# Performance work log

Hardware: AMD Instinct MI355X
Metric: run time of the kernel (lower is better)

The kernel has to match this reference:

```python
import jax, jax.numpy as jnp
import numpy as np
import math

B, T = 16, 512
P = 256          # num_memory_positions
E = 128          # embedding_dim
NB = 4           # num_beings
K = 4            # attention_radius
TEMP = 8.0       # attention_temperature
PHI = 1.618033988749895


def setup_inputs() -> dict:
    key = jax.random.key(0)
    ks = jax.random.split(key, 8)
    x = jax.random.normal(ks[0], (B, T, 8), jnp.float32)
    W_in = jax.random.normal(ks[1], (8, E), jnp.float32) * 0.1
    b_in = jnp.zeros((E,), jnp.float32)
    W_out = jax.random.normal(ks[2], (E, 8), jnp.float32) * 0.1
    b_out = jnp.zeros((8,), jnp.float32)
    W_p = jax.random.normal(ks[3], (E, E), jnp.float32) * (1.0 / np.sqrt(E))
    b_p = jnp.zeros((E,), jnp.float32)
    ptr_dest = jax.random.uniform(ks[4], (NB, P), jnp.float32) * P
    jump_W = jax.random.normal(ks[5], (NB, E), jnp.float32) * 0.1
    jump_b = jnp.zeros((NB,), jnp.float32)
    ctx_strength = jnp.full((NB,), 0.2, jnp.float32)
    pe = np.zeros((NB, E), np.float32)
    for i in range(NB):
        ph = i * PHI
        v = []
        for h in range(1, 9):
            v += [math.sin(h * ph), math.cos(h * ph)]
        pe[i, :16] = v  # phase_embedding padded with zeros to E (E >= 16)
    phase_bias = jnp.asarray(pe)
    seg = P / NB
    pointer_init = jax.random.uniform(ks[6], (NB, B), jnp.float32) * seg + jnp.arange(NB, dtype=jnp.float32)[:, None] * seg
    return dict(x=x, W_in=W_in, b_in=b_in, W_out=W_out, b_out=b_out,
                W_p=W_p, b_p=b_p, ptr_dest=ptr_dest, jump_W=jump_W,
                jump_b=jump_b, ctx_strength=ctx_strength,
                phase_bias=phase_bias, pointer_init=pointer_init)


def _forward(x, W_in, b_in, W_out, b_out, W_p, b_p, ptr_dest, jump_W,
             jump_b, ctx_strength, phase_bias, pointer_init):
    offsets = jnp.arange(-K, K + 1)          # [W]
    b_ix = jnp.arange(B)                     # [B]
    half = P / 2.0
    ring0 = jnp.zeros((B, P, E), x.dtype)
    hid0 = jnp.zeros((NB, B, E), x.dtype)

    def step(carry, x_t):
        ring, ptrs, hids = carry
        inp = x_t @ W_in + b_in              # [B,E]
        outs, new_ptrs, new_hids = [], [], []
        for i in range(NB):                  # beings sequential (share ring)
            ptr, hid = ptrs[i], hids[i]
            base = jnp.clip(jnp.floor(ptr).astype(jnp.int32), 0, P - 1)
            idx = (base[:, None] + offsets[None, :]) % P            # [B,W]
            delta = jnp.mod(idx.astype(x_t.dtype) - ptr[:, None] + half, P) - half
            w = jax.nn.softmax(-(delta ** 2) / TEMP, axis=1)         # [B,W]
            nbhd = ring[b_ix[:, None], idx]                          # [B,W,E]
            ctx = jnp.sum(w[..., None] * nbhd, axis=1)               # [B,E]
            comb = inp + jax.nn.sigmoid(ctx_strength[i]) * ctx + 0.1 * phase_bias[i]
            s = jnp.tanh(comb + hid)
            s = jnp.tanh(s @ W_p + b_p)      # depth-1 = 1 processing layer
            ring = ring.at[b_ix[:, None], idx].add(w[..., None] * s[:, None, :])
            cur = jnp.clip(ptr.astype(jnp.int32), 0, P - 1)
            jump_target = ptr_dest[i][cur]                           # [B]
            probs = jax.nn.sigmoid(s @ jump_W[i] + jump_b[i])        # [B]
            hard = (probs > 0.5).astype(s.dtype)
            should_jump = hard - jax.lax.stop_gradient(probs) + probs
            walk = (ptr + 1.0) % P
            new_ptrs.append(jnp.where(should_jump > 0.5, jump_target, walk))
            new_hids.append(s)
            outs.append(s @ W_out + b_out)                           # [B,8]
        out_t = jnp.mean(jnp.stack(outs), axis=0)                    # [B,8] (training-mode mean)
        return (ring, jnp.stack(new_ptrs), jnp.stack(new_hids)), out_t

    _, ys = jax.lax.scan(step, (ring0, pointer_init, hid0), jnp.swapaxes(x, 0, 1))
    return jnp.swapaxes(ys, 0, 1)            # [B,T,8]


def reference(x, W_in, b_in, W_out, b_out, W_p, b_p, ptr_dest, jump_W,
              jump_b, ctx_strength, phase_bias, pointer_init):
    return _forward(x, W_in, b_in, W_out, b_out, W_p, b_p, ptr_dest,
                    jump_W, jump_b, ctx_strength, phase_bias, pointer_init)
```

## Files before the change

kernel.cpp:

```cpp
#include <hip/hip_runtime.h>
#include <cmath>

namespace {
constexpr int B_ = 16, T_ = 512, P_ = 256, E_ = 128, NB_ = 4, K_ = 4;
constexpr int THREADS_ = 512;
constexpr int RS_ = 132;

__device__ __forceinline__ float rcpf(float x) { return __builtin_amdgcn_rcpf(x); }
__device__ __forceinline__ float fast_tanh(float x) {
    float a = fabsf(x);
    float t = __expf(-2.0f * a);
    float r = 1.0f - 2.0f * t * rcpf(1.0f + t);
    return copysignf(r, x);
}

__device__ __forceinline__ void lgkm_barrier() {
    __builtin_amdgcn_sched_barrier(0);
    asm volatile("s_waitcnt lgkmcnt(0)\n\ts_barrier" ::: "memory");
    __builtin_amdgcn_sched_barrier(0);
}

template<int CTRL>
__device__ __forceinline__ float dpp_addf(float v) {
    const int s = __builtin_amdgcn_update_dpp(0, __float_as_int(v), CTRL, 0xF, 0xF, true);
    return v + __int_as_float(s);
}
template<int Q>
__device__ __forceinline__ float dpp_bcast4(float v) {
    const int s = __builtin_amdgcn_update_dpp(0, __float_as_int(v), Q * 0x55, 0xF, 0xF, true);
    return __int_as_float(s);
}
__device__ __forceinline__ float pl16_sum(float v) {
#if __has_builtin(__builtin_amdgcn_permlane16_swap)
    const unsigned u = __float_as_uint(v);
    const auto r = __builtin_amdgcn_permlane16_swap(u, u, false, false);
    return __uint_as_float(r[0]) + __uint_as_float(r[1]);
#else
    return v + __shfl_xor(v, 16);
#endif
}
__device__ __forceinline__ float pl32_sum(float v) {
#if __has_builtin(__builtin_amdgcn_permlane32_swap)
    const unsigned u = __float_as_uint(v);
    const auto r = __builtin_amdgcn_permlane32_swap(u, u, false, false);
    return __uint_as_float(r[0]) + __uint_as_float(r[1]);
#else
    return v + __shfl_xor(v, 32);
#endif
}
__device__ __forceinline__ float redkq8(float v) {
    v = dpp_addf<0x128>(v);
    v = pl16_sum(v);
    v = pl32_sum(v);
    return v;
}
__device__ __forceinline__ float redpair(float v) {
    v = dpp_addf<0xB1>(v);
    v = dpp_addf<0x4E>(v);
    v = dpp_addf<0x141>(v);
    return v;
}
__device__ __forceinline__ float sel8f(int kq, float w0, float w1, float w2, float w3,
                                       float w4, float w5, float w6, float w7) {
    const float a = (kq & 1) ? w1 : w0;
    const float b = (kq & 1) ? w3 : w2;
    const float c = (kq & 1) ? w5 : w4;
    const float d = (kq & 1) ? w7 : w6;
    const float e = (kq & 2) ? b : a;
    const float f = (kq & 2) ? d : c;
    return (kq & 4) ? f : e;
}
}

__global__ __launch_bounds__(512, 1)
void swarm_ring_kernel(const float* __restrict__ x,
                       const float* __restrict__ W_in,
                       const float* __restrict__ b_in,
                       const float* __restrict__ W_out,
                       const float* __restrict__ b_out,
                       const float* __restrict__ W_p,
                       const float* __restrict__ b_p,
                       const float* __restrict__ ptr_dest,
                       const float* __restrict__ jump_W,
                       const float* __restrict__ jump_b,
                       const float* __restrict__ ctx_strength,
                       const float* __restrict__ phase_bias,
                       const float* __restrict__ pointer_init,
                       float* __restrict__ out)
{
    __shared__ alignas(16) float  ring[P_ * RS_];
    __shared__ alignas(16) float4 s4[136];
    __shared__ alignas(16) float  sbuf[2][160];
    __shared__ alignas(16) float  red[32];
    __shared__ alignas(16) float  hist[16][132];
    __shared__ alignas(16) float  wout_s[8][132];

    const int tid = threadIdx.x;
    const int b   = blockIdx.x;
    const int w   = tid >> 6;
    const int l   = tid & 63;
    const int s_  = l & 7;
    const int kq  = l >> 3;
    const int e0  = ((w << 3) | s_) << 1;

    for (int k4 = tid; k4 < P_ * RS_ / 4; k4 += THREADS_)
        ((float4*)ring)[k4] = make_float4(0.f, 0.f, 0.f, 0.f);
    for (int idx = tid; idx < 8 * E_; idx += THREADS_) {
        const int m = idx >> 7, ee = idx & 127;
        wout_s[m][ee] = W_out[ee * 8 + m] * 0.25f;
    }

    float2 wp2[16];
    #pragma unroll
    for (int kk = 0; kk < 16; ++kk)
        wp2[kk] = *(const float2*)(W_p + (kq * 16 + kk) * E_ + e0);

    float2 wi2[8];
    #pragma unroll
    for (int k = 0; k < 8; ++k)
        wi2[k] = *(const float2*)(W_in + k * E_ + e0);

    const float2 bin2 = *(const float2*)(b_in + e0);
    const float2 bp2  = *(const float2*)(b_p + e0);
    const float  bout_m = b_out[tid & 7];

    float2 pb2[NB_], jw2[NB_], hid2[NB_];
    float  sigc[NB_], jb_r[NB_], ptrv[NB_];
    #pragma unroll
    for (int i = 0; i < NB_; ++i) {
        const float2 pb = *(const float2*)(phase_bias + i * E_ + e0);
        pb2[i] = make_float2(0.1f * pb.x, 0.1f * pb.y);
        jw2[i] = *(const float2*)(jump_W + i * E_ + e0);
        sigc[i] = 1.0f / (1.0f + __expf(-ctx_strength[i]));
        jb_r[i] = jump_b[i];
        hid2[i] = make_float2(0.f, 0.f);
        ptrv[i] = pointer_init[i * B_ + b];
    }

    const float* xb = x + (size_t)b * T_ * 8;
    float xt[8];
    {
        float4 a0 = ((const float4*)xb)[0], a1 = ((const float4*)xb)[1];
        xt[0]=a0.x; xt[1]=a0.y; xt[2]=a0.z; xt[3]=a0.w;
        xt[4]=a1.x; xt[5]=a1.y; xt[6]=a1.z; xt[7]=a1.w;
    }

    const float Cw1 = 0.8824969f, Cw2 = 0.60653066f, Cw3 = 0.32465247f, Cw4 = 0.13533528f;
    const float Dw1 = 0.7788008f, Dw2 = 0.36787944f, Dw3 = 0.105399225f, Dw4 = 0.018315639f;

    __syncthreads();

    for (int t = 0; t < T_; ++t) {
        int   baseA[NB_];
        float fA[NB_], psinv[NB_], jt[NB_], wgt[NB_][9];
        #pragma unroll
        for (int i = 0; i < NB_; ++i) {
            const float p = ptrv[i];
            const int base = (int)p;
            baseA[i] = base;
            jt[i] = ptr_dest[i * P_ + base];
            const float f = p - (float)base;
            fA[i] = f;
            const float r  = __expf(0.25f * f);
            const float r2 = r * r, r3 = r2 * r, r4 = r2 * r2;
            const float ri = rcpf(r), ri2 = ri * ri, ri3 = ri2 * ri, ri4 = ri2 * ri2;
            const float p0 = Cw4*ri4, p1 = Cw3*ri3, p2 = Cw2*ri2, p3 = Cw1*ri, p4 = 1.0f,
                        p5 = Cw1*r,  p6 = Cw2*r2,  p7 = Cw3*r3,  p8 = Cw4*r4;
            const float sum = ((p0+p1)+(p2+p3)) + ((p4+p5)+(p6+p7)) + p8;
            const float inv = rcpf(sum);
            psinv[i] = inv;
            wgt[i][0]=p0*inv; wgt[i][1]=p1*inv; wgt[i][2]=p2*inv; wgt[i][3]=p3*inv;
            wgt[i][4]=p4*inv; wgt[i][5]=p5*inv; wgt[i][6]=p6*inv; wgt[i][7]=p7*inv;
            wgt[i][8]=p8*inv;
        }

        int ddm[NB_][NB_];
        bool overlap = false;
        #pragma unroll
        for (int j = 1; j < NB_; ++j)
            #pragma unroll
            for (int i = 0; i < j; ++i) {
                const int dd = ((baseA[j] - baseA[i] + 128) & 255) - 128;
                ddm[j][i] = dd;
                overlap = overlap || (dd >= -8 && dd <= 8);
            }

        float  ws[NB_], w8[NB_];
        float2 ctxp2[NB_];
        #pragma unroll
        for (int i = 0; i < NB_; ++i) {
            ws[i] = sel8f(kq, wgt[i][0], wgt[i][1], wgt[i][2], wgt[i][3],
                              wgt[i][4], wgt[i][5], wgt[i][6], wgt[i][7]);
            w8[i] = wgt[i][8];
            const int r0 = (baseA[i] + kq - K_) & (P_ - 1);
            const float2 g0 = *(const float2*)(ring + r0 * RS_ + e0);
            float cx = ws[i] * g0.x;
            float cy = ws[i] * g0.y;
            if (kq == 0) {
                const int r2 = (baseA[i] + K_) & (P_ - 1);
                const float2 g2 = *(const float2*)(ring + r2 * RS_ + e0);
                cx = fmaf(w8[i], g2.x, cx);
                cy = fmaf(w8[i], g2.y, cy);
            }
            ctxp2[i] = make_float2(redkq8(cx), redkq8(cy));
        }

        float2 inp2 = bin2;
        #pragma unroll
        for (int k = 0; k < 8; ++k) {
            inp2.x = fmaf(xt[k], wi2[k].x, inp2.x);
            inp2.y = fmaf(xt[k], wi2[k].y, inp2.y);
        }

        float xtn[8];
        if (t + 1 < T_) {
            float4 a0 = ((const float4*)(xb + (t + 1) * 8))[0];
            float4 a1 = ((const float4*)(xb + (t + 1) * 8))[1];
            xtn[0]=a0.x; xtn[1]=a0.y; xtn[2]=a0.z; xtn[3]=a0.w;
            xtn[4]=a1.x; xtn[5]=a1.y; xtn[6]=a1.z; xtn[7]=a1.w;
        } else {
            #pragma unroll
            for (int k = 0; k < 8; ++k) xtn[k] = 0.f;
        }

        float2 sv2[NB_];

        if (!overlap) {
            float2 s1v[NB_];
            #pragma unroll
            for (int j = 0; j < NB_; ++j) {
                s1v[j].x = fast_tanh(fmaf(sigc[j], ctxp2[j].x, inp2.x + pb2[j].x + hid2[j].x));
                s1v[j].y = fast_tanh(fmaf(sigc[j], ctxp2[j].y, inp2.y + pb2[j].y + hid2[j].y));
            }
            if (kq == 0) {
                const int si = 17 * w + (s_ << 1);
                s4[si]     = make_float4(s1v[0].x, s1v[1].x, s1v[2].x, s1v[3].x);
                s4[si + 1] = make_float4(s1v[0].y, s1v[1].y, s1v[2].y, s1v[3].y);
            }
            lgkm_barrier();

            float2 ab0 = make_float2(0.f, 0.f), ab1 = ab0, ab2 = ab0, ab3 = ab0;
            const float4* sp = s4 + kq * 17;
            #pragma unroll
            for (int kk = 0; kk < 16; ++kk) {
                const float4 sq = sp[kk];
                const float2 w2 = wp2[kk];
                ab0.x = fmaf(sq.x, w2.x, ab0.x); ab0.y = fmaf(sq.x, w2.y, ab0.y);
                ab1.x = fmaf(sq.y, w2.x, ab1.x); ab1.y = fmaf(sq.y, w2.y, ab1.y);
                ab2.x = fmaf(sq.z, w2.x, ab2.x); ab2.y = fmaf(sq.z, w2.y, ab2.y);
                ab3.x = fmaf(sq.w, w2.x, ab3.x); ab3.y = fmaf(sq.w, w2.y, ab3.y);
            }
            sv2[0] = make_float2(fast_tanh(redkq8(ab0.x) + bp2.x), fast_tanh(redkq8(ab0.y) + bp2.y));
            sv2[1] = make_float2(fast_tanh(redkq8(ab1.x) + bp2.x), fast_tanh(redkq8(ab1.y) + bp2.y));
            sv2[2] = make_float2(fast_tanh(redkq8(ab2.x) + bp2.x), fast_tanh(redkq8(ab2.y) + bp2.y));
            sv2[3] = make_float2(fast_tanh(redkq8(ab3.x) + bp2.x), fast_tanh(redkq8(ab3.y) + bp2.y));
            #pragma unroll
            for (int j = 0; j < NB_; ++j) hid2[j] = sv2[j];

            #pragma unroll
            for (int j = 0; j < NB_; ++j) {
                const float2 s = sv2[j];
                const int r0 = (baseA[j] + kq - K_) & (P_ - 1);
                float2* q0 = (float2*)(ring + r0 * RS_ + e0);
                float2 v0 = *q0;
                v0.x = fmaf(ws[j], s.x, v0.x); v0.y = fmaf(ws[j], s.y, v0.y);
                *q0 = v0;
                if (kq == 0) {
                    const int r2 = (baseA[j] + K_) & (P_ - 1);
                    float2* q2 = (float2*)(ring + r2 * RS_ + e0);
                    float2 v2 = *q2;
                    v2.x = fmaf(w8[j], s.x, v2.x); v2.y = fmaf(w8[j], s.y, v2.y);
                    *q2 = v2;
                }
            }
        } else {
            float coefm[NB_][NB_];
            #pragma unroll
            for (int j = 1; j < NB_; ++j) {
                #pragma unroll
                for (int i = 0; i < j; ++i) {
                    const int dd = ddm[j][i];
                    float c = 0.f;
                    if (dd >= -8 && dd <= 8) {
                        const float A = (float)dd - fA[i];
                        const float s  = __expf(-0.25f * (A - fA[j]));
                        const float G  = __expf(0.125f * (fA[i] * fA[i] - A * A));
                        const float s2p = s * s, s3p = s2p * s, s4p = s2p * s2p;
                        const float si = rcpf(s), si2 = si * si, si3 = si2 * si, si4 = si2 * si2;
                        float acc = 0.f;
                        acc += (dd >= 0)              ? Dw4 * si4 : 0.f;
                        acc += (dd >= -1 && dd <= 7)  ? Dw3 * si3 : 0.f;
                        acc += (dd >= -2 && dd <= 6)  ? Dw2 * si2 : 0.f;
                        acc += (dd >= -3 && dd <= 5)  ? Dw1 * si  : 0.f;
                        acc += (dd >= -4 && dd <= 4)  ? 1.0f      : 0.f;
                        acc += (dd >= -5 && dd <= 3)  ? Dw1 * s   : 0.f;
                        acc += (dd >= -6 && dd <= 2)  ? Dw2 * s2p : 0.f;
                        acc += (dd >= -7 && dd <= 1)  ? Dw3 * s3p : 0.f;
                        acc += (dd <= 0)              ? Dw4 * s4p : 0.f;
                        c = psinv[i] * psinv[j] * G * acc;
                    }
                    coefm[j][i] = c;
                }
            }

            #pragma unroll
            for (int j = 0; j < NB_; ++j) {
                float2 ctx = ctxp2[j];
                #pragma unroll
                for (int i = 0; i < j; ++i) {
                    ctx.x = fmaf(coefm[j][i], sv2[i].x, ctx.x);
                    ctx.y = fmaf(coefm[j][i], sv2[i].y, ctx.y);
                }
                float2 s1;
                s1.x = fast_tanh(fmaf(sigc[j], ctx.x, inp2.x + pb2[j].x + hid2[j].x));
                s1.y = fast_tanh(fmaf(sigc[j], ctx.y, inp2.y + pb2[j].y + hid2[j].y));
                if (kq == 0) {
                    const int pf = 20 * w + (s_ << 1);
                    *(float2*)(&sbuf[j & 1][pf]) = s1;
                }
                lgkm_barrier();

                const float4* sp4 = (const float4*)(&sbuf[j & 1][0]);
                float ax = 0.f, ay = 0.f;
                #pragma unroll
                for (int m = 0; m < 4; ++m) {
                    const float4 sq = sp4[5 * kq + m];
                    const float2 wa = wp2[4*m+0], wb = wp2[4*m+1];
                    const float2 wc = wp2[4*m+2], wd = wp2[4*m+3];
                    ax = fmaf(sq.x, wa.x, ax); ay = fmaf(sq.x, wa.y, ay);
                    ax = fmaf(sq.y, wb.x, ax); ay = fmaf(sq.y, wb.y, ay);
                    ax = fmaf(sq.z, wc.x, ax); ay = fmaf(sq.z, wc.y, ay);
                    ax = fmaf(sq.w, wd.x, ax); ay = fmaf(sq.w, wd.y, ay);
                }
                float2 s2;
                s2.x = fast_tanh(redkq8(ax) + bp2.x);
                s2.y = fast_tanh(redkq8(ay) + bp2.y);
                sv2[j] = s2; hid2[j] = s2;

                const int r0 = (baseA[j] + kq - K_) & (P_ - 1);
                float2* q0 = (float2*)(ring + r0 * RS_ + e0);
                float2 v0 = *q0;
                v0.x = fmaf(ws[j], s2.x, v0.x); v0.y = fmaf(ws[j], s2.y, v0.y);
                *q0 = v0;
                if (kq == 0) {
                    const int r2 = (baseA[j] + K_) & (P_ - 1);
                    float2* q2 = (float2*)(ring + r2 * RS_ + e0);
                    float2 v2 = *q2;
                    v2.x = fmaf(w8[j], s2.x, v2.x); v2.y = fmaf(w8[j], s2.y, v2.y);
                    *q2 = v2;
                }
            }
        }

        {
            float vj0 = fmaf(sv2[0].y, jw2[0].y, sv2[0].x * jw2[0].x);
            float vj1 = fmaf(sv2[1].y, jw2[1].y, sv2[1].x * jw2[1].x);
            float vj2 = fmaf(sv2[2].y, jw2[2].y, sv2[2].x * jw2[2].x);
            float vj3 = fmaf(sv2[3].y, jw2[3].y, sv2[3].x * jw2[3].x);
            vj0 = redpair(vj0); vj1 = redpair(vj1); vj2 = redpair(vj2); vj3 = redpair(vj3);
            if (l == 0)
                ((float4*)red)[w] = make_float4(vj0, vj1, vj2, vj3);
        }

        {
            float2 ssum2;
            ssum2.x = (sv2[0].x + sv2[1].x) + (sv2[2].x + sv2[3].x);
            ssum2.y = (sv2[0].y + sv2[1].y) + (sv2[2].y + sv2[3].y);
            if (kq == 0) *(float2*)(&hist[t & 15][e0]) = ssum2;
        }

        lgkm_barrier();

        {
            float rv = red[l & 31];
            rv = dpp_addf<0x124>(rv);
            rv = dpp_addf<0x128>(rv);
            rv = pl16_sum(rv);
            const float zz0 = dpp_bcast4<0>(rv) + jb_r[0];
            const float zz1 = dpp_bcast4<1>(rv) + jb_r[1];
            const float zz2 = dpp_bcast4<2>(rv) + jb_r[2];
            const float zz3 = dpp_bcast4<3>(rv) + jb_r[3];
            const float zz[4] = { zz0, zz1, zz2, zz3 };
            #pragma unroll
            for (int i = 0; i < NB_; ++i) {
                float np;
                if (zz[i] > 0.0f) np = jt[i];
                else { np = ptrv[i] + 1.0f; if (np >= 256.0f) np -= 256.0f; }
                ptrv[i] = np;
            }
        }

        if ((t & 7) == 7 && tid < 64) {
            const int tt = tid >> 3;
            const int m  = tid & 7;
            const float* hrow = hist[(t - 7 + tt) & 15];
            const float* wrow = wout_s[m];
            float acc = 0.f;
            #pragma unroll
            for (int q = 0; q < 32; ++q) {
                const float4 h4 = ((const float4*)hrow)[q];
                const float4 w4 = ((const float4*)wrow)[q];
                acc += ((h4.x * w4.x + h4.y * w4.y) + (h4.z * w4.z + h4.w * w4.w));
            }
            out[((size_t)b * T_ + (t - 7 + tt)) * 8 + m] = acc + bout_m;
        }

        #pragma unroll
        for (int k = 0; k < 8; ++k) xt[k] = xtn[k];
    }
}

extern "C" void kernel_launch(void* const* d_in, const int* in_sizes, int n_in,
                              void* d_out, int out_size, void* d_ws, size_t ws_size,
                              hipStream_t stream) {
    (void)in_sizes; (void)n_in; (void)out_size; (void)d_ws; (void)ws_size;
    swarm_ring_kernel<<<dim3(B_), dim3(THREADS_), 0, stream>>>(
        (const float*)d_in[0],  (const float*)d_in[1],  (const float*)d_in[2],
        (const float*)d_in[3],  (const float*)d_in[4],  (const float*)d_in[5],
        (const float*)d_in[6],  (const float*)d_in[7],  (const float*)d_in[8],
        (const float*)d_in[9],  (const float*)d_in[10], (const float*)d_in[11],
        (const float*)d_in[12], (float*)d_out);
}
```

Baseline: 2.035 ms.

## Compute W_p projection with bf16x3-split MFMA instead of scalar FMAs

```diff
diff --git a/kernel.cpp b/kernel.cpp
--- a/kernel.cpp
+++ b/kernel.cpp
@@ -5,6 +5,10 @@
 constexpr int B_ = 16, T_ = 512, P_ = 256, E_ = 128, NB_ = 4, K_ = 4;
 constexpr int THREADS_ = 512;
 constexpr int RS_ = 132;
+
+typedef __attribute__((ext_vector_type(8))) short        bf16x8;
+typedef __attribute__((ext_vector_type(4))) float        f32x4;
+typedef __attribute__((ext_vector_type(4))) unsigned int u32x4;
 
 __device__ __forceinline__ float rcpf(float x) { return __builtin_amdgcn_rcpf(x); }
 __device__ __forceinline__ float fast_tanh(float x) {
@@ -18,6 +22,27 @@
     __builtin_amdgcn_sched_barrier(0);
     asm volatile("s_waitcnt lgkmcnt(0)\n\ts_barrier" ::: "memory");
     __builtin_amdgcn_sched_barrier(0);
+}
+
+__device__ __forceinline__ unsigned bf16rn_hi(float x) {
+    const unsigned u = __float_as_uint(x);
+    return (u + 0x7FFFu + ((u >> 16) & 1u)) & 0xFFFF0000u;
+}
+__device__ __forceinline__ void split3_pack(float x, float y,
+                                            unsigned &hp, unsigned &mp, unsigned &lp) {
+    const unsigned xh = bf16rn_hi(x);
+    const float    xr1 = x - __uint_as_float(xh);
+    const unsigned xm = bf16rn_hi(xr1);
+    const float    xr2 = xr1 - __uint_as_float(xm);
+    const unsigned xl = bf16rn_hi(xr2);
+    const unsigned yh = bf16rn_hi(y);
+    const float    yr1 = y - __uint_as_float(yh);
+    const unsigned ym = bf16rn_hi(yr1);
+    const float    yr2 = yr1 - __uint_as_float(ym);
+    const unsigned yl = bf16rn_hi(yr2);
+    hp = (xh >> 16) | yh;
+    mp = (xm >> 16) | ym;
+    lp = (xl >> 16) | yl;
 }
 
 template<int CTRL>
@@ -59,6 +84,11 @@
     v = dpp_addf<0x4E>(v);
     v = dpp_addf<0x141>(v);
     return v;
+}
+__device__ __forceinline__ float sel4(int q, float a, float b, float c, float d) {
+    const float t0 = (q & 1) ? b : a;
+    const float t1 = (q & 1) ? d : c;
+    return (q & 2) ? t1 : t0;
 }
 __device__ __forceinline__ float sel8f(int kq, float w0, float w1, float w2, float w3,
                                        float w4, float w5, float w6, float w7) {
@@ -88,12 +118,11 @@
                        const float* __restrict__ pointer_init,
                        float* __restrict__ out)
 {
-    __shared__ alignas(16) float  ring[P_ * RS_];
-    __shared__ alignas(16) float4 s4[136];
-    __shared__ alignas(16) float  sbuf[2][160];
-    __shared__ alignas(16) float  red[32];
-    __shared__ alignas(16) float  hist[16][132];
-    __shared__ alignas(16) float  wout_s[8][132];
+    __shared__ alignas(16) float    ring[P_ * RS_];
+    __shared__ alignas(16) unsigned s1Tp[4][3][68];
+    __shared__ alignas(16) float    red[32];
+    __shared__ alignas(16) float    hist[16][132];
+    __shared__ alignas(16) float    wout_s[8][132];
 
     const int tid = threadIdx.x;
     const int b   = blockIdx.x;
@@ -102,6 +131,10 @@
     const int s_  = l & 7;
     const int kq  = l >> 3;
     const int e0  = ((w << 3) | s_) << 1;
+    const int pr  = (w << 3) | s_;
+    const int g   = l >> 4;
+    const int arow = l & 3;
+    const int ecol = (w << 4) | (l & 15);
 
     for (int k4 = tid; k4 < P_ * RS_ / 4; k4 += THREADS_)
         ((float4*)ring)[k4] = make_float4(0.f, 0.f, 0.f, 0.f);
@@ -109,11 +142,26 @@
         const int m = idx >> 7, ee = idx & 127;
         wout_s[m][ee] = W_out[ee * 8 + m] * 0.25f;
     }
-
-    float2 wp2[16];
+    for (int i2 = tid; i2 < 4 * 3 * 68; i2 += THREADS_)
+        ((unsigned*)s1Tp)[i2] = 0u;
+
+    bf16x8 bh[4], bm[4], bl[4];
     #pragma unroll
-    for (int kk = 0; kk < 16; ++kk)
-        wp2[kk] = *(const float2*)(W_p + (kq * 16 + kk) * E_ + e0);
+    for (int ks = 0; ks < 4; ++ks) {
+        u32x4 uh, um, ul;
+        #pragma unroll
+        for (int p = 0; p < 4; ++p) {
+            const int k0 = 32 * ks + 8 * g + 2 * p;
+            const float w0 = W_p[(size_t)k0 * E_ + ecol];
+            const float w1 = W_p[(size_t)(k0 + 1) * E_ + ecol];
+            unsigned hp, mp, lp;
+            split3_pack(w0, w1, hp, mp, lp);
+            uh[p] = hp; um[p] = mp; ul[p] = lp;
+        }
+        bh[ks] = __builtin_bit_cast(bf16x8, uh);
+        bm[ks] = __builtin_bit_cast(bf16x8, um);
+        bl[ks] = __builtin_bit_cast(bf16x8, ul);
+    }
 
     float2 wi2[8];
     #pragma unroll
@@ -121,7 +169,7 @@
         wi2[k] = *(const float2*)(W_in + k * E_ + e0);
 
     const float2 bin2 = *(const float2*)(b_in + e0);
-    const float2 bp2  = *(const float2*)(b_p + e0);
+    const float  bpc  = b_p[ecol];
     const float  bout_m = b_out[tid & 7];
 
     float2 pb2[NB_], jw2[NB_], hid2[NB_];
@@ -232,28 +280,41 @@
                 s1v[j].x = fast_tanh(fmaf(sigc[j], ctxp2[j].x, inp2.x + pb2[j].x + hid2[j].x));
                 s1v[j].y = fast_tanh(fmaf(sigc[j], ctxp2[j].y, inp2.y + pb2[j].y + hid2[j].y));
             }
-            if (kq == 0) {
-                const int si = 17 * w + (s_ << 1);
-                s4[si]     = make_float4(s1v[0].x, s1v[1].x, s1v[2].x, s1v[3].x);
-                s4[si + 1] = make_float4(s1v[0].y, s1v[1].y, s1v[2].y, s1v[3].y);
+            {
+                const float sx = sel4(kq, s1v[0].x, s1v[1].x, s1v[2].x, s1v[3].x);
+                const float sy = sel4(kq, s1v[0].y, s1v[1].y, s1v[2].y, s1v[3].y);
+                unsigned hp, mp, lp;
+                split3_pack(sx, sy, hp, mp, lp);
+                if (kq < 4) {
+                    s1Tp[kq][0][pr] = hp;
+                    s1Tp[kq][1][pr] = mp;
+                    s1Tp[kq][2][pr] = lp;
+                }
             }
             lgkm_barrier();
 
-            float2 ab0 = make_float2(0.f, 0.f), ab1 = ab0, ab2 = ab0, ab3 = ab0;
-            const float4* sp = s4 + kq * 17;
-            #pragma unroll
-            for (int kk = 0; kk < 16; ++kk) {
-                const float4 sq = sp[kk];
-                const float2 w2 = wp2[kk];
-                ab0.x = fmaf(sq.x, w2.x, ab0.x); ab0.y = fmaf(sq.x, w2.y, ab0.y);
-                ab1.x = fmaf(sq.y, w2.x, ab1.x); ab1.y = fmaf(sq.y, w2.y, ab1.y);
-                ab2.x = fmaf(sq.z, w2.x, ab2.x); ab2.y = fmaf(sq.z, w2.y, ab2.y);
-                ab3.x = fmaf(sq.w, w2.x, ab3.x); ab3.y = fmaf(sq.w, w2.y, ab3.y);
-            }
-            sv2[0] = make_float2(fast_tanh(redkq8(ab0.x) + bp2.x), fast_tanh(redkq8(ab0.y) + bp2.y));
-            sv2[1] = make_float2(fast_tanh(redkq8(ab1.x) + bp2.x), fast_tanh(redkq8(ab1.y) + bp2.y));
-            sv2[2] = make_float2(fast_tanh(redkq8(ab2.x) + bp2.x), fast_tanh(redkq8(ab2.y) + bp2.y));
-            sv2[3] = make_float2(fast_tanh(redkq8(ab3.x) + bp2.x), fast_tanh(redkq8(ab3.y) + bp2.y));
+            f32x4 accA = {0.f,0.f,0.f,0.f}, accB = accA, accC = accA;
+            #pragma unroll
+            for (int ks = 0; ks < 4; ++ks) {
+                const bf16x8 ah = *(const bf16x8*)&s1Tp[arow][0][16 * ks + 4 * g];
+                const bf16x8 am = *(const bf16x8*)&s1Tp[arow][1][16 * ks + 4 * g];
+                const bf16x8 al = *(const bf16x8*)&s1Tp[arow][2][16 * ks + 4 * g];
+                accA = __builtin_amdgcn_mfma_f32_16x16x32_bf16(ah, bh[ks], accA, 0, 0, 0);
+                accB = __builtin_amdgcn_mfma_f32_16x16x32_bf16(ah, bm[ks], accB, 0, 0, 0);
+                accB = __builtin_amdgcn_mfma_f32_16x16x32_bf16(am, bh[ks], accB, 0, 0, 0);
+                accC = __builtin_amdgcn_mfma_f32_16x16x32_bf16(ah, bl[ks], accC, 0, 0, 0);
+                accC = __builtin_amdgcn_mfma_f32_16x16x32_bf16(am, bm[ks], accC, 0, 0, 0);
+                accC = __builtin_amdgcn_mfma_f32_16x16x32_bf16(al, bh[ks], accC, 0, 0, 0);
+            }
+            const float t0 = fast_tanh(((accB[0] + accC[0]) + accA[0]) + bpc);
+            const float t1 = fast_tanh(((accB[1] + accC[1]) + accA[1]) + bpc);
+            const float t2 = fast_tanh(((accB[2] + accC[2]) + accA[2]) + bpc);
+            const float t3 = fast_tanh(((accB[3] + accC[3]) + accA[3]) + bpc);
+            const int sl0 = s_ << 1, sl1 = sl0 + 1;
+            sv2[0] = make_float2(__shfl(t0, sl0), __shfl(t0, sl1));
+            sv2[1] = make_float2(__shfl(t1, sl0), __shfl(t1, sl1));
+            sv2[2] = make_float2(__shfl(t2, sl0), __shfl(t2, sl1));
+            sv2[3] = make_float2(__shfl(t3, sl0), __shfl(t3, sl1));
             #pragma unroll
             for (int j = 0; j < NB_; ++j) hid2[j] = sv2[j];
 
@@ -314,27 +375,37 @@
                 float2 s1;
                 s1.x = fast_tanh(fmaf(sigc[j], ctx.x, inp2.x + pb2[j].x + hid2[j].x));
                 s1.y = fast_tanh(fmaf(sigc[j], ctx.y, inp2.y + pb2[j].y + hid2[j].y));
-                if (kq == 0) {
-                    const int pf = 20 * w + (s_ << 1);
-                    *(float2*)(&sbuf[j & 1][pf]) = s1;
+                {
+                    unsigned hp, mp, lp;
+                    split3_pack(s1.x, s1.y, hp, mp, lp);
+                    if (kq == 0) {
+                        s1Tp[j][0][pr] = hp;
+                        s1Tp[j][1][pr] = mp;
+                        s1Tp[j][2][pr] = lp;
+                    }
                 }
                 lgkm_barrier();
 
-                const float4* sp4 = (const float4*)(&sbuf[j & 1][0]);
-                float ax = 0.f, ay = 0.f;
+                f32x4 accA = {0.f,0.f,0.f,0.f}, accB = accA, accC = accA;
                 #pragma unroll
-                for (int m = 0; m < 4; ++m) {
-                    const float4 sq = sp4[5 * kq + m];
-                    const float2 wa = wp2[4*m+0], wb = wp2[4*m+1];
-                    const float2 wc = wp2[4*m+2], wd = wp2[4*m+3];
-                    ax = fmaf(sq.x, wa.x, ax); ay = fmaf(sq.x, wa.y, ay);
-                    ax = fmaf(sq.y, wb.x, ax); ay = fmaf(sq.y, wb.y, ay);
-                    ax = fmaf(sq.z, wc.x, ax); ay = fmaf(sq.z, wc.y, ay);
-                    ax = fmaf(sq.w, wd.x, ax); ay = fmaf(sq.w, wd.y, ay);
-                }
-                float2 s2;
-                s2.x = fast_tanh(redkq8(ax) + bp2.x);
-                s2.y = fast_tanh(redkq8(ay) + bp2.y);
+                for (int ks = 0; ks < 4; ++ks) {
+                    const bf16x8 ah = *(const bf16x8*)&s1Tp[arow][0][16 * ks + 4 * g];
+                    const bf16x8 am = *(const bf16x8*)&s1Tp[arow][1][16 * ks + 4 * g];
+                    const bf16x8 al = *(const bf16x8*)&s1Tp[arow][2][16 * ks + 4 * g];
+                    accA = __builtin_amdgcn_mfma_f32_16x16x32_bf16(ah, bh[ks], accA, 0, 0, 0);
+                    accB = __builtin_amdgcn_mfma_f32_16x16x32_bf16(ah, bm[ks], accB, 0, 0, 0);
+                    accB = __builtin_amdgcn_mfma_f32_16x16x32_bf16(am, bh[ks], accB, 0, 0, 0);
+                    accC = __builtin_amdgcn_mfma_f32_16x16x32_bf16(ah, bl[ks], accC, 0, 0, 0);
+                    accC = __builtin_amdgcn_mfma_f32_16x16x32_bf16(am, bm[ks], accC, 0, 0, 0);
+                    accC = __builtin_amdgcn_mfma_f32_16x16x32_bf16(al, bh[ks], accC, 0, 0, 0);
+                }
+                float tj;
+                if (j == 0)      tj = fast_tanh(((accB[0] + accC[0]) + accA[0]) + bpc);
+                else if (j == 1) tj = fast_tanh(((accB[1] + accC[1]) + accA[1]) + bpc);
+                else if (j == 2) tj = fast_tanh(((accB[2] + accC[2]) + accA[2]) + bpc);
+                else             tj = fast_tanh(((accB[3] + accC[3]) + accA[3]) + bpc);
+                const int sl0 = s_ << 1;
+                float2 s2 = make_float2(__shfl(tj, sl0), __shfl(tj, sl0 + 1));
                 sv2[j] = s2; hid2[j] = s2;
 
                 const int r0 = (baseA[j] + kq - K_) & (P_ - 1);
```

Result: slower. 2.322 ms (+14.1%).
